# Performance work log

Measured on AMD Instinct MI355X. Metric: run time of the kernel, lower is better.

The kernel has to match this reference:

```python
import jax, jax.numpy as jnp
import numpy as np

EPSILON = 0.001  # clip margin from HParams.epsilon
_EPS32 = float(np.finfo(np.float32).eps)  # added to bound in create_ops


@jax.custom_jvp
def floor_ste(x):
    """Floor with Straight-Through-Estimator gradient."""
    return jnp.floor(x)


@floor_ste.defjvp
def _floor_ste_jvp(primals, tangents):
    (x,), (t,) = primals, tangents
    return jnp.floor(x), t


def _binarize(x, bound):
    # (-inf,0) -> -bound/2, [0,inf) -> +bound/2, via scale-clip-floor-STE
    scale = 1.0 / bound
    clip_bound = 1.0 - EPSILON
    y = jnp.clip(x * scale, -clip_bound, clip_bound)
    y = floor_ste(y) + 0.5
    return (y / scale).astype(x.dtype)


def setup_inputs() -> dict:
    key = jax.random.key(0)
    k1, k2 = jax.random.split(key, 2)
    B, S, D, F = 4, 4096, 2048, 8192
    inputs = jax.random.normal(k1, (B, S, D), dtype=jnp.float32)
    # lecun_normal init: std = 1/sqrt(fan_in)
    kernel = jax.random.normal(k2, (D, F), dtype=jnp.float32) * (1.0 / np.sqrt(D))
    bias = jnp.zeros((F,), dtype=jnp.float32)
    return {"inputs": inputs, "kernel": kernel, "bias": bias}


def reference(inputs, kernel, bias):
    # weight bound: max |W| over contraction axes (axis 0), shape (1, F)
    w_bound = jax.lax.stop_gradient(
        jnp.max(jnp.abs(kernel), axis=0, keepdims=True) + _EPS32)
    k_bin = _binarize(kernel, w_bound)
    # input bound: max |x| over contraction axis (last), per-row, shape (B, S, 1)
    a_bound = jax.lax.stop_gradient(
        jnp.max(jnp.abs(inputs), axis=-1, keepdims=True) + _EPS32)
    x_bin = _binarize(inputs, a_bound)
    out = jnp.einsum('bsd,df->bsf', x_bin, k_bin)  # [B, S, F]
    return out + bias
```

## Files before the change

kernel.cpp:

```cpp
#include <hip/hip_runtime.h>
#include <stdint.h>

#define MDIM 16384
#define NDIM 8192
#define KDIM 2048
#define KB2 1024
#define EPS32 1.1920928955078125e-07f
#define BM 256
#define BN 256

using i32x4 = __attribute__((ext_vector_type(4))) int;
using i32x8 = __attribute__((ext_vector_type(8))) int;
using f32x4 = __attribute__((ext_vector_type(4))) float;
using f32x16 = __attribute__((ext_vector_type(16))) float;
typedef __attribute__((address_space(3))) const int8_t* lds_cptr;
typedef __attribute__((address_space(3))) int8_t* lds_ptr;

__device__ __forceinline__ uint32_t nib(float v) { return (v < 0.f) ? 0xAu : 0x2u; }

__global__ __launch_bounds__(256) void k_pack(const float* __restrict__ x,
                                              const float* __restrict__ W,
                                              uint8_t* __restrict__ As,
                                              uint8_t* __restrict__ Bs,
                                              float* __restrict__ ab,
                                              unsigned int* __restrict__ wbu) {
  __shared__ uint8_t sm[64 * 68];
  __shared__ float red[4][64];
  const int t = threadIdx.x;
  if (blockIdx.x < MDIM) {
    const int m = blockIdx.x;
    const float4* row = (const float4*)(x + (size_t)m * KDIM);
    const float4 v0 = row[2 * t];
    const float4 v1 = row[2 * t + 1];
    const uint32_t pk =
        nib(v0.x) | (nib(v0.y) << 4) | (nib(v0.z) << 8) | (nib(v0.w) << 12) |
        (nib(v1.x) << 16) | (nib(v1.y) << 20) | (nib(v1.z) << 24) | (nib(v1.w) << 28);
    ((uint32_t*)(As + (size_t)m * KB2))[t] = pk;
    float mx = fmaxf(fmaxf(fabsf(v0.x), fabsf(v0.y)), fmaxf(fabsf(v0.z), fabsf(v0.w)));
    mx = fmaxf(mx, fmaxf(fmaxf(fabsf(v1.x), fabsf(v1.y)), fmaxf(fabsf(v1.z), fabsf(v1.w))));
#pragma unroll
    for (int o = 32; o > 0; o >>= 1) mx = fmaxf(mx, __shfl_xor(mx, o, 64));
    if ((t & 63) == 0) red[0][t >> 6] = mx;
    __syncthreads();
    if (t == 0)
      ab[m] = fmaxf(fmaxf(red[0][0], red[0][1]), fmaxf(red[0][2], red[0][3])) + EPS32;
  } else {
    const int bid = blockIdx.x - MDIM;
    const int bd = bid & 31;
    const int bf = bid >> 5;
    const int d0 = bd * 64, f0 = bf * 64;
    const int fl = t & 63, dq = t >> 6;
    float mx = 0.f;
#pragma unroll
    for (int i = 0; i < 16; ++i) {
      const int dl = i * 4 + dq;
      const float v = W[(size_t)(d0 + dl) * NDIM + f0 + fl];
      sm[fl * 68 + dl] = (uint8_t)nib(v);
      mx = fmaxf(mx, fabsf(v));
    }
    red[dq][fl] = mx;
    __syncthreads();
    if (t < 64) {
      const float r = fmaxf(fmaxf(red[0][t], red[1][t]), fmaxf(red[2][t], red[3][t]));
      atomicMax(&wbu[f0 + t], __float_as_uint(r));
    }
    const int nl = t >> 2, ch = t & 3;
    const uint8_t* s = &sm[nl * 68 + ch * 16];
    uint32_t w0 = 0, w1 = 0;
#pragma unroll
    for (int i = 0; i < 4; ++i)
      w0 |= (uint32_t)(s[2 * i] | (s[2 * i + 1] << 4)) << (8 * i);
#pragma unroll
    for (int i = 0; i < 4; ++i)
      w1 |= (uint32_t)(s[8 + 2 * i] | (s[9 + 2 * i] << 4)) << (8 * i);
    *(uint2*)(Bs + (size_t)(f0 + nl) * KB2 + (d0 >> 1) + ch * 8) = make_uint2(w0, w1);
  }
}

__global__ __launch_bounds__(512, 2) void k_gemm(const uint8_t* __restrict__ As,
                                                 const uint8_t* __restrict__ Bs,
                                                 const float* __restrict__ ab,
                                                 const float* __restrict__ wbf,
                                                 const float* __restrict__ bias,
                                                 float* __restrict__ out) {
  __shared__ int8_t lds[4][32768];
  const int t = threadIdx.x;
  const int lane = t & 63, wid = t >> 6;
  const int bid = blockIdx.x;
  const int xcd = bid & 7;
  const int local = bid >> 3;
  const int bnin = local & 7;
  const int bml = (local >> 3) & 7;
  const int bnc = local >> 6;
  const int bm = xcd * 8 + bml;
  const int bn = bnc * 8 + bnin;
  const size_t m0 = (size_t)bm * BM, n0 = (size_t)bn * BN;
  const int wr = wid >> 2, wc = wid & 3;

  const int r4 = lane >> 2;
  const int c4 = lane & 3;
  const uint8_t* glA0 = As + (m0 + (size_t)(wid * 32 + r4)) * KB2 + c4 * 16;
  const uint8_t* glA1 = As + (m0 + (size_t)(wid * 32 + 16 + r4)) * KB2 + c4 * 16;
  const uint8_t* glB0 = Bs + (n0 + (size_t)(wid * 32 + r4)) * KB2 + c4 * 16;
  const uint8_t* glB1 = Bs + (n0 + (size_t)(wid * 32 + 16 + r4)) * KB2 + c4 * 16;
  const int xs0 = (lane >> 5) & 1;
  const int wsl0 = (c4 ^ xs0) * 16;
  const int wsl1 = (c4 ^ (xs0 ^ 2)) * 16;
  const int wrowA0 = (wid * 32 + r4) * 64 + wsl0;
  const int wrowA1 = (wid * 32 + 16 + r4) * 64 + wsl1;

  const int l31 = lane & 31, h = lane >> 5;
  const int xs = (l31 >> 3) & 3;
  const int aoff0 = (wr * 128 + l31) * 64 + ((h ^ xs) * 16);
  const int aoff1 = (wr * 128 + l31) * 64 + (((2 + h) ^ xs) * 16);
  const int boff0 = 16384 + (wc * 64 + l31) * 64 + ((h ^ xs) * 16);
  const int boff1 = 16384 + (wc * 64 + l31) * 64 + (((2 + h) ^ xs) * 16);

  f32x16 acc[4][2];
#pragma unroll
  for (int i = 0; i < 4; ++i)
#pragma unroll
    for (int j = 0; j < 2; ++j) acc[i][j] = (f32x16){0};

  i32x4 sE0, sE1, sE2, sE3, sO0, sO1, sO2, sO3;

#define GLOAD(dst, p) \
  asm volatile("global_load_dwordx4 %0, %1, off" : "=v"(dst) : "v"(p))

#define GL4(u, S0, S1, S2, S3)                  \
  do {                                          \
    GLOAD(S0, glA0 + (size_t)(u) * 64);         \
    GLOAD(S1, glA1 + (size_t)(u) * 64);         \
    GLOAD(S2, glB0 + (size_t)(u) * 64);         \
    GLOAD(S3, glB1 + (size_t)(u) * 64);         \
  } while (0)

#define DSW(addr, val, OFF) \
  asm volatile("ds_write_b128 %0, %1 offset:" #OFF :: "v"(addr), "v"(val))

#define WR4(u, S0, S1, S2, S3)                              \
  do {                                                      \
    lds_ptr w0 = (lds_ptr)&lds[(u) & 3][0] + wrowA0;        \
    lds_ptr w1 = (lds_ptr)&lds[(u) & 3][0] + wrowA1;        \
    DSW(w0, S0, 0);                                         \
    DSW(w1, S1, 0);                                         \
    DSW(w0, S2, 16384);                                     \
    DSW(w1, S3, 16384);                                     \
  } while (0)

#define VMW(N)                                              \
  asm volatile("s_waitcnt vmcnt(" #N ")" ::: "memory");     \
  __builtin_amdgcn_sched_barrier(0);

#define DSR(dst, ptr, OFF) \
  asm volatile("ds_read_b128 %0, %1 offset:" #OFF : "=v"(dst) : "v"(ptr))

#define LGK(N)                                              \
  asm volatile("s_waitcnt lgkmcnt(" #N ")" ::: "memory");   \
  __builtin_amdgcn_sched_barrier(0);

#define FR(x) __builtin_shufflevector((x), (x), 0, 1, 2, 3, -1, -1, -1, -1)

#define SMFMA(D, FB, FA)                                                      \
  D = __builtin_amdgcn_mfma_scale_f32_32x32x64_f8f6f4(                        \
      (FB), (FA), D, 4, 4, 0, 0x7F7F7F7F, 0, 0x7F7F7F7F)

#define MP2(I, FB0, FB1, FA) SMFMA(acc[I][0], FB0, FA); SMFMA(acc[I][1], FB1, FA)

#define LADDER(SLOT)                                                          \
  {                                                                           \
    const int8_t* sb = &lds[(SLOT)][0];                                       \
    lds_cptr pA0 = (lds_cptr)(sb + aoff0);                                    \
    lds_cptr pA1 = (lds_cptr)(sb + aoff1);                                    \
    lds_cptr pB0 = (lds_cptr)(sb + boff0);                                    \
    lds_cptr pB1 = (lds_cptr)(sb + boff1);                                    \
    i32x4 a0, a1, a2, a3, a4, a5, a6, a7, b0, b1, b2, b3;                     \
    DSR(a0, pA0, 0); DSR(b0, pB0, 0); DSR(b1, pB0, 2048);                     \
    DSR(a1, pA0, 2048); DSR(a2, pA0, 4096); DSR(a3, pA0, 6144);               \
    DSR(a4, pA1, 0); DSR(b2, pB1, 0); DSR(b3, pB1, 2048);                     \
    DSR(a5, pA1, 2048); DSR(a6, pA1, 4096); DSR(a7, pA1, 6144);               \
    LGK(9);                                                                   \
    i32x8 FB0 = FR(b0), FB1 = FR(b1), FA = FR(a0);                            \
    __builtin_amdgcn_s_setprio(1); MP2(0, FB0, FB1, FA);                      \
    LGK(8); FA = FR(a1); MP2(1, FB0, FB1, FA);                                \
    LGK(7); FA = FR(a2); MP2(2, FB0, FB1, FA);                                \
    LGK(6); FA = FR(a3); MP2(3, FB0, FB1, FA);                                \
    LGK(3); FB0 = FR(b2); FB1 = FR(b3); FA = FR(a4); MP2(0, FB0, FB1, FA);    \
    LGK(2); FA = FR(a5); MP2(1, FB0, FB1, FA);                                \
    LGK(1); FA = FR(a6); MP2(2, FB0, FB1, FA);                                \
    LGK(0); FA = FR(a7); MP2(3, FB0, FB1, FA);                                \
    __builtin_amdgcn_s_setprio(0);                                            \
  }

#define ITER_EVEN(TT, DOLOAD, VMN)                                            \
  {                                                                           \
    __builtin_amdgcn_s_barrier();                                             \
    if (DOLOAD) GL4((TT) + 3, sO0, sO1, sO2, sO3);                            \
    VMW(VMN);                                                                 \
    WR4((TT) + 2, sE0, sE1, sE2, sE3);                                        \
    LADDER((TT) & 3);                                                         \
  }
#define ITER_ODD(TT, DOLOAD, VMN)                                             \
  {                                                                           \
    __builtin_amdgcn_s_barrier();                                             \
    if (DOLOAD) GL4((TT) + 3, sE0, sE1, sE2, sE3);                            \
    VMW(VMN);                                                                 \
    WR4((TT) + 2, sO0, sO1, sO2, sO3);                                        \
    LADDER((TT) & 3);                                                         \
  }

  GL4(0, sE0, sE1, sE2, sE3);
  VMW(0);
  WR4(0, sE0, sE1, sE2, sE3);
  GL4(1, sO0, sO1, sO2, sO3);
  VMW(0);
  WR4(1, sO0, sO1, sO2, sO3);
  asm volatile("s_waitcnt lgkmcnt(0)" ::: "memory");
  GL4(2, sE0, sE1, sE2, sE3);

  for (int tt = 0; tt < 12; tt += 2) {
    ITER_EVEN(tt, 1, 4);
    ITER_ODD(tt + 1, 1, 4);
  }
  ITER_EVEN(12, 1, 4);
  ITER_ODD(13, 0, 0);
  { __builtin_amdgcn_s_barrier(); LADDER(2); }
  { __builtin_amdgcn_s_barrier(); LADDER(3); }

#pragma unroll
  for (int i = 0; i < 4; ++i) {
    const size_t m = m0 + wr * 128 + i * 32 + l31;
    const float av = 0.25f * ab[m];
    float* orow = out + m * NDIM;
#pragma unroll
    for (int j = 0; j < 2; ++j) {
#pragma unroll
      for (int q = 0; q < 4; ++q) {
        const size_t nb = n0 + wc * 64 + j * 32 + q * 8 + h * 4;
        const f32x4 wv = *(const f32x4*)&wbf[nb];
        const f32x4 bv = *(const f32x4*)&bias[nb];
        f32x4 o;
        o[0] = av * ((wv[0] + EPS32) * acc[i][j][q * 4 + 0]) + bv[0];
        o[1] = av * ((wv[1] + EPS32) * acc[i][j][q * 4 + 1]) + bv[1];
        o[2] = av * ((wv[2] + EPS32) * acc[i][j][q * 4 + 2]) + bv[2];
        o[3] = av * ((wv[3] + EPS32) * acc[i][j][q * 4 + 3]) + bv[3];
        *(f32x4*)(orow + nb) = o;
      }
    }
  }
#undef ITER_EVEN
#undef ITER_ODD
#undef LADDER
#undef MP2
#undef SMFMA
#undef FR
#undef LGK
#undef DSR
#undef VMW
#undef WR4
#undef DSW
#undef GL4
#undef GLOAD
}

extern "C" void kernel_launch(void* const* d_in, const int* in_sizes, int n_in,
                              void* d_out, int out_size, void* d_ws, size_t ws_size,
                              hipStream_t stream) {
  const float* x = (const float*)d_in[0];
  const float* W = (const float*)d_in[1];
  const float* bias = (const float*)d_in[2];
  float* out = (float*)d_out;

  char* ws = (char*)d_ws;
  uint8_t* As = (uint8_t*)ws;
  uint8_t* Bs = (uint8_t*)(ws + (size_t)(16u << 20));
  float* ab = (float*)(ws + (size_t)(24u << 20));
  float* wb = (float*)(ws + (size_t)(24u << 20) + (1u << 16));

  (void)hipMemsetAsync(wb, 0, NDIM * sizeof(float), stream);
  k_pack<<<MDIM + (KDIM / 64) * (NDIM / 64), 256, 0, stream>>>(x, W, As, Bs, ab,
                                                               (unsigned int*)wb);
  k_gemm<<<(MDIM / BM) * (NDIM / BN), 512, 0, stream>>>(As, Bs, ab, wb, bias, out);
}
```

Baseline: 303.5 us.

## Restructure main loop into two-tile super-iterations with one barrier each

Replaces the per-k-tile pipeline (one barrier per tile, loads issued three tiles ahead with partial vmcnt waits) with super-steps. Each super-step issues global loads for two future tiles, runs two MFMA ladders, then waits, writes both tiles to LDS and hits a single barrier. This halves the number of workgroup barriers. In exchange the prefetch distance shrinks, global loads must fully complete at the end of each super-step, and the LDS writes now sit on the critical path before the barrier instead of overlapping with compute.

```diff
diff --git a/kernel.cpp b/kernel.cpp
--- a/kernel.cpp
+++ b/kernel.cpp
@@ -127,12 +127,16 @@
 #define GLOAD(dst, p) \
   asm volatile("global_load_dwordx4 %0, %1, off" : "=v"(dst) : "v"(p))
 
-#define GL4(u, S0, S1, S2, S3)                  \
-  do {                                          \
-    GLOAD(S0, glA0 + (size_t)(u) * 64);         \
-    GLOAD(S1, glA1 + (size_t)(u) * 64);         \
-    GLOAD(S2, glB0 + (size_t)(u) * 64);         \
-    GLOAD(S3, glB1 + (size_t)(u) * 64);         \
+#define GL8(u)                                      \
+  do {                                              \
+    GLOAD(sE0, glA0 + (size_t)(u) * 64);            \
+    GLOAD(sE1, glA1 + (size_t)(u) * 64);            \
+    GLOAD(sE2, glB0 + (size_t)(u) * 64);            \
+    GLOAD(sE3, glB1 + (size_t)(u) * 64);            \
+    GLOAD(sO0, glA0 + (size_t)((u) + 1) * 64);      \
+    GLOAD(sO1, glA1 + (size_t)((u) + 1) * 64);      \
+    GLOAD(sO2, glB0 + (size_t)((u) + 1) * 64);      \
+    GLOAD(sO3, glB1 + (size_t)((u) + 1) * 64);      \
   } while (0)
 
 #define DSW(addr, val, OFF) \
@@ -146,6 +150,12 @@
     DSW(w1, S1, 0);                                         \
     DSW(w0, S2, 16384);                                     \
     DSW(w1, S3, 16384);                                     \
+  } while (0)
+
+#define WR8(u)                                              \
+  do {                                                      \
+    WR4((u), sE0, sE1, sE2, sE3);                           \
+    WR4((u) + 1, sO0, sO1, sO2, sO3);                       \
   } while (0)
 
 #define VMW(N)                                              \
@@ -192,40 +202,28 @@
     __builtin_amdgcn_s_setprio(0);                                            \
   }
 
-#define ITER_EVEN(TT, DOLOAD, VMN)                                            \
+#define SUPER(S, DOLOAD)                                                      \
   {                                                                           \
+    if (DOLOAD) GL8(2 * (S) + 2);                                             \
+    LADDER((2 * (S)) & 3);                                                    \
+    LADDER((2 * (S) + 1) & 3);                                                \
+    if (DOLOAD) {                                                             \
+      VMW(0);                                                                 \
+      WR8(2 * (S) + 2);                                                       \
+      asm volatile("s_waitcnt lgkmcnt(0)" ::: "memory");                      \
+    }                                                                         \
     __builtin_amdgcn_s_barrier();                                             \
-    if (DOLOAD) GL4((TT) + 3, sO0, sO1, sO2, sO3);                            \
-    VMW(VMN);                                                                 \
-    WR4((TT) + 2, sE0, sE1, sE2, sE3);                                        \
-    LADDER((TT) & 3);                                                         \
-  }
-#define ITER_ODD(TT, DOLOAD, VMN)                                             \
-  {                                                                           \
-    __builtin_amdgcn_s_barrier();                                             \
-    if (DOLOAD) GL4((TT) + 3, sE0, sE1, sE2, sE3);                            \
-    VMW(VMN);                                                                 \
-    WR4((TT) + 2, sO0, sO1, sO2, sO3);                                        \
-    LADDER((TT) & 3);                                                         \
-  }
-
-  GL4(0, sE0, sE1, sE2, sE3);
+  }
+
+  GL8(0);
   VMW(0);
-  WR4(0, sE0, sE1, sE2, sE3);
-  GL4(1, sO0, sO1, sO2, sO3);
-  VMW(0);
-  WR4(1, sO0, sO1, sO2, sO3);
+  WR8(0);
   asm volatile("s_waitcnt lgkmcnt(0)" ::: "memory");
-  GL4(2, sE0, sE1, sE2, sE3);
-
-  for (int tt = 0; tt < 12; tt += 2) {
-    ITER_EVEN(tt, 1, 4);
-    ITER_ODD(tt + 1, 1, 4);
-  }
-  ITER_EVEN(12, 1, 4);
-  ITER_ODD(13, 0, 0);
-  { __builtin_amdgcn_s_barrier(); LADDER(2); }
-  { __builtin_amdgcn_s_barrier(); LADDER(3); }
+  __builtin_amdgcn_s_barrier();
+
+#pragma unroll 2
+  for (int s = 0; s < 7; ++s) SUPER(s, 1);
+  SUPER(7, 0);
 
 #pragma unroll
   for (int i = 0; i < 4; ++i) {
@@ -248,8 +246,7 @@
       }
     }
   }
-#undef ITER_EVEN
-#undef ITER_ODD
+#undef SUPER
 #undef LADDER
 #undef MP2
 #undef SMFMA
@@ -257,9 +254,10 @@
 #undef LGK
 #undef DSR
 #undef VMW
+#undef WR8
 #undef WR4
 #undef DSW
-#undef GL4
+#undef GL8
 #undef GLOAD
 }
 
```

Result: slower. 317.1 us (+4.5%).
